# Optimization experiments

Measured on AMD Instinct MI355X. Metric: run time of the kernel, lower is better.

Reference implementation:

```python
import jax, jax.numpy as jnp
import numpy as np

N = 50000   # nodes
E = 800000  # edges (before self-loops)
IN = 128; H = 4; C = 32; HC = H * C; OUT = 47
EPS = 1e-16  # PyG softmax denominator eps
NEG_SLOPE = 0.2


def setup_inputs() -> dict:
    key = jax.random.key(0)
    ks = jax.random.split(key, 20)
    g = lambda k, shape, s=0.1: (jax.random.normal(k, shape, dtype=jnp.float32) * s)
    inp = {}
    inp["x"] = jax.random.normal(ks[0], (N, IN), dtype=jnp.float32)
    inp["edge_index"] = jax.random.randint(ks[1], (2, E), 0, N, dtype=jnp.int32)
    # layer 0: GATConv(IN -> H*C, concat=True) + skip Linear(IN -> HC)
    inp["lin_w0"] = g(ks[2], (IN, HC)); inp["att_src0"] = g(ks[3], (H, C)); inp["att_dst0"] = g(ks[4], (H, C))
    inp["bias0"] = g(ks[5], (HC,)); inp["skip_w0"] = g(ks[6], (IN, HC)); inp["skip_b0"] = g(ks[7], (HC,))
    # layer 1: GATConv(HC -> H*C, concat=True) + skip Linear(HC -> HC)
    inp["lin_w1"] = g(ks[8], (HC, HC)); inp["att_src1"] = g(ks[9], (H, C)); inp["att_dst1"] = g(ks[10], (H, C))
    inp["bias1"] = g(ks[11], (HC,)); inp["skip_w1"] = g(ks[12], (HC, HC)); inp["skip_b1"] = g(ks[13], (HC,))
    # layer 2: GATConv(HC -> OUT, heads=H, concat=False) + skip Linear(HC -> OUT)
    inp["lin_w2"] = g(ks[14], (HC, H * OUT)); inp["att_src2"] = g(ks[15], (H, OUT)); inp["att_dst2"] = g(ks[16], (H, OUT))
    inp["bias2"] = g(ks[17], (OUT,)); inp["skip_w2"] = g(ks[18], (HC, OUT)); inp["skip_b2"] = g(ks[19], (OUT,))
    return inp


def _gat_conv(x, src, dst, lin_w, att_src, att_dst, bias, concat):
    """PyG GATConv (self-loops already appended to src/dst)."""
    h, c = att_src.shape
    n = x.shape[0]
    xh = (x @ lin_w).reshape(n, h, c)                      # [N, H, C]
    a_src = jnp.einsum('nhc,hc->nh', xh, att_src)          # [N, H]
    a_dst = jnp.einsum('nhc,hc->nh', xh, att_dst)          # [N, H]
    e = a_src[src] + a_dst[dst]                            # [E', H]
    e = jax.nn.leaky_relu(e, NEG_SLOPE)
    # segment softmax over incoming edges per destination node
    m = jax.ops.segment_max(e, dst, num_segments=n)        # [N, H]
    ex = jnp.exp(e - m[dst])
    s = jax.ops.segment_sum(ex, dst, num_segments=n)       # [N, H]
    alpha = ex / (s[dst] + EPS)                            # [E', H]
    out = jax.ops.segment_sum(xh[src] * alpha[:, :, None], dst, num_segments=n)  # [N, H, C]
    out = out.reshape(n, h * c) if concat else out.mean(axis=1)
    return out + bias


def reference(x, edge_index, lin_w0, att_src0, att_dst0, bias0, skip_w0, skip_b0,
              lin_w1, att_src1, att_dst1, bias1, skip_w1, skip_b1,
              lin_w2, att_src2, att_dst2, bias2, skip_w2, skip_b2):
    n = x.shape[0]
    loop = jnp.arange(n, dtype=edge_index.dtype)
    src = jnp.concatenate([edge_index[0], loop])
    dst = jnp.concatenate([edge_index[1], loop])
    # layer 0 (+ skip, ELU; dropout is identity at inference)
    x = _gat_conv(x, src, dst, lin_w0, att_src0, att_dst0, bias0, True) + x @ skip_w0 + skip_b0
    x = jax.nn.elu(x)
    # layer 1
    x = _gat_conv(x, src, dst, lin_w1, att_src1, att_dst1, bias1, True) + x @ skip_w1 + skip_b1
    x = jax.nn.elu(x)
    # layer 2 (concat=False -> head mean), no activation
    x = _gat_conv(x, src, dst, lin_w2, att_src2, att_dst2, bias2, False) + x @ skip_w2 + skip_b2
    return x
```

## Files before the change

kernel.cpp:

```cpp
#include <hip/hip_runtime.h>
#include <math.h>
#include <type_traits>

#define KD 128
#define HC 128
#define NF2 188
#define NF2P 192
#define OUTC 47

typedef __attribute__((ext_vector_type(8))) __bf16 bf16x8;
typedef __attribute__((ext_vector_type(2))) __bf16 bf16x2;
typedef __attribute__((ext_vector_type(4))) float f32x4;

#ifdef __has_builtin
#if __has_builtin(__builtin_amdgcn_fdot2_f32_bf16)
#define HAVE_FDOT2 1
#endif
#endif

__device__ inline float bfhi_to_f(unsigned int u) {
    union { unsigned int u; float f; } c; c.u = u & 0xFFFF0000u; return c.f;
}
__device__ inline float bflo_to_f(unsigned int u) {
    union { unsigned int u; float f; } c; c.u = u << 16; return c.f;
}
__device__ inline unsigned short f_to_bfu(float f) {
    return __builtin_bit_cast(unsigned short, (__bf16)f);
}
__device__ inline unsigned int pk_bf(float a, float b) {
    return (unsigned int)f_to_bfu(a) | ((unsigned int)f_to_bfu(b) << 16);
}
__device__ inline float dot2pair(uint2 q, uint2 ab, float acc) {
#ifdef HAVE_FDOT2
    acc = __builtin_amdgcn_fdot2_f32_bf16(__builtin_bit_cast(bf16x2, q.x),
                                          __builtin_bit_cast(bf16x2, ab.x), acc, false);
    acc = __builtin_amdgcn_fdot2_f32_bf16(__builtin_bit_cast(bf16x2, q.y),
                                          __builtin_bit_cast(bf16x2, ab.y), acc, false);
#else
    acc += bflo_to_f(q.x) * bflo_to_f(ab.x) + bfhi_to_f(q.x) * bfhi_to_f(ab.x);
    acc += bflo_to_f(q.y) * bflo_to_f(ab.y) + bfhi_to_f(q.y) * bfhi_to_f(ab.y);
#endif
    return acc;
}

__global__ void init_deg_kernel(int* deg, int* counter, int n) {
    int i = blockIdx.x * blockDim.x + threadIdx.x;
    if (i < n) deg[i] = 1;
    if (i == 0) *counter = 0;
}

__global__ void count_kernel(const int* __restrict__ dst, int* deg, int e) {
    int t = blockIdx.x * blockDim.x + threadIdx.x;
    int base = t * 8;
    if (base + 7 < e) {
        int4 d0 = *(const int4*)(dst + base);
        int4 d1 = *(const int4*)(dst + base + 4);
        atomicAdd(&deg[d0.x], 1); atomicAdd(&deg[d0.y], 1);
        atomicAdd(&deg[d0.z], 1); atomicAdd(&deg[d0.w], 1);
        atomicAdd(&deg[d1.x], 1); atomicAdd(&deg[d1.y], 1);
        atomicAdd(&deg[d1.z], 1); atomicAdd(&deg[d1.w], 1);
    } else {
        for (int k = base; k < e; ++k) atomicAdd(&deg[dst[k]], 1);
    }
}

__global__ __launch_bounds__(256) void scan_base_kernel(
    const int* __restrict__ deg, int* counter,
    int* __restrict__ row_ptr, int* __restrict__ fill, int* __restrict__ col, int n) {
    int i = blockIdx.x * 256 + threadIdx.x;
    int v = (i < n) ? deg[i] : 0;
    int lane = threadIdx.x & 63, w = threadIdx.x >> 6;
    int incl = v;
#pragma unroll
    for (int off = 1; off < 64; off <<= 1) {
        int u = __shfl_up(incl, off, 64);
        if (lane >= off) incl += u;
    }
    __shared__ int wsum[4];
    __shared__ int base_sh;
    if (lane == 63) wsum[w] = incl;
    __syncthreads();
    if (threadIdx.x == 0)
        base_sh = atomicAdd(counter, wsum[0] + wsum[1] + wsum[2] + wsum[3]);
    int woff = 0;
    for (int k = 0; k < w; ++k) woff += wsum[k];
    __syncthreads();
    int excl = base_sh + woff + incl - v;
    if (i < n) {
        row_ptr[i] = excl;
        col[excl] = i;
        fill[i] = excl + 1;
    }
}

__global__ void fill_kernel(const int* __restrict__ ei, int* fill, int* col, int e) {
    int t = blockIdx.x * blockDim.x + threadIdx.x;
    int base = t * 8;
    if (base + 7 < e) {
        int4 s0 = *(const int4*)(ei + base);
        int4 s1 = *(const int4*)(ei + base + 4);
        int4 d0 = *(const int4*)(ei + e + base);
        int4 d1 = *(const int4*)(ei + e + base + 4);
        int p0 = atomicAdd(&fill[d0.x], 1);
        int p1 = atomicAdd(&fill[d0.y], 1);
        int p2 = atomicAdd(&fill[d0.z], 1);
        int p3 = atomicAdd(&fill[d0.w], 1);
        int p4 = atomicAdd(&fill[d1.x], 1);
        int p5 = atomicAdd(&fill[d1.y], 1);
        int p6 = atomicAdd(&fill[d1.z], 1);
        int p7 = atomicAdd(&fill[d1.w], 1);
        col[p0] = s0.x; col[p1] = s0.y; col[p2] = s0.z; col[p3] = s0.w;
        col[p4] = s1.x; col[p5] = s1.y; col[p6] = s1.z; col[p7] = s1.w;
    } else {
        for (int k = base; k < e; ++k) {
            int pos = atomicAdd(&fill[ei[e + k]], 1);
            col[pos] = ei[k];
        }
    }
}

template <typename AT, int NLIN, int NSK, int TR>
__global__ __launch_bounds__(256) void gemm_fused_kernel(
    const AT* __restrict__ A,
    const float* __restrict__ B0, __bf16* __restrict__ out0, int N0, int ldc0,
    const float* __restrict__ B1, const float* __restrict__ bias1,
    float* __restrict__ out1, int N1, int M) {
    __shared__ __bf16 As[64][136];
    __shared__ __bf16 Bs[64][136];
    int tid = threadIdx.x;
    int m0 = blockIdx.x * 64;

#pragma unroll
    for (int rep = 0; rep < 4; ++rep) {
        int idx = tid + rep * 256;
        int row = idx >> 4, seg = idx & 15;
        int gm = m0 + row;
        bf16x8 v = {};
        if (gm < M) {
            if constexpr (std::is_same<AT, float>::value) {
                const float* p = A + gm * KD + seg * 8;
                float4 f0 = *(const float4*)p;
                float4 f1 = *(const float4*)(p + 4);
                v[0] = (__bf16)f0.x; v[1] = (__bf16)f0.y; v[2] = (__bf16)f0.z; v[3] = (__bf16)f0.w;
                v[4] = (__bf16)f1.x; v[5] = (__bf16)f1.y; v[6] = (__bf16)f1.z; v[7] = (__bf16)f1.w;
            } else {
                v = *(const bf16x8*)(A + gm * KD + seg * 8);
            }
        }
        *(bf16x8*)&As[row][seg * 8] = v;
    }
    __syncthreads();

    int w = tid >> 6, lane = tid & 63;
    int lr = lane & 15, quad = lane >> 4;

#pragma unroll
    for (int t = 0; t < NLIN + NSK; ++t) {
        bool second = t >= NLIN;
        const float* B = second ? B1 : B0;
        int N = second ? N1 : N0;
        int n0 = (second ? (t - NLIN) : t) * 64;
        if (t) __syncthreads();
#pragma unroll
        for (int rep = 0; rep < 4; ++rep) {
            int idx = tid + rep * 256;
            int n = idx & 63, seg = idx >> 6;
            bf16x8 v = {};
            if (n0 + n < N) {
#pragma unroll
                for (int i = 0; i < 8; ++i) v[i] = (__bf16)B[(seg * 8 + i) * N + n0 + n];
            }
            *(bf16x8*)&Bs[n][seg * 8] = v;
        }
        __syncthreads();

        f32x4 acc[4] = {};
#pragma unroll
        for (int kc = 0; kc < 128; kc += 32) {
            bf16x8 a0 = *(const bf16x8*)&As[w * 16 + lr][kc + quad * 8];
            bf16x8 b0 = *(const bf16x8*)&Bs[lr][kc + quad * 8];
            bf16x8 b1 = *(const bf16x8*)&Bs[16 + lr][kc + quad * 8];
            bf16x8 b2 = *(const bf16x8*)&Bs[32 + lr][kc + quad * 8];
            bf16x8 b3 = *(const bf16x8*)&Bs[48 + lr][kc + quad * 8];
            acc[0] = __builtin_amdgcn_mfma_f32_16x16x32_bf16(a0, b0, acc[0], 0, 0, 0);
            acc[1] = __builtin_amdgcn_mfma_f32_16x16x32_bf16(a0, b1, acc[1], 0, 0, 0);
            acc[2] = __builtin_amdgcn_mfma_f32_16x16x32_bf16(a0, b2, acc[2], 0, 0, 0);
            acc[3] = __builtin_amdgcn_mfma_f32_16x16x32_bf16(a0, b3, acc[3], 0, 0, 0);
        }
#pragma unroll
        for (int c = 0; c < 4; ++c) {
#pragma unroll
            for (int reg = 0; reg < 4; ++reg) {
                int row = m0 + w * 16 + quad * 4 + reg;
                int colg = n0 + c * 16 + lr;
                if (row < M && colg < N) {
                    float v = acc[c][reg];
                    if (second) {
                        if (bias1) v += bias1[colg];
                        out1[row * N + colg] = v;
                    } else {
                        int idx;
                        if (TR) {
                            int h = (colg * 1395) >> 16;
                            idx = row * ldc0 + (colg - 47 * h) * 4 + h;
                        } else {
                            idx = row * ldc0 + colg;
                        }
                        out0[idx] = (__bf16)v;
                    }
                }
            }
        }
    }
}

__global__ __launch_bounds__(256) void att_kernel(
    const __bf16* __restrict__ xh, const float* __restrict__ att_s,
    const float* __restrict__ att_d, float* __restrict__ a_src,
    float* __restrict__ a_dst, int n) {
    int node = (blockIdx.x * blockDim.x + threadIdx.x) >> 6;
    int lane = threadIdx.x & 63;
    if (node >= n) return;
    float hs[4] = {0.f, 0.f, 0.f, 0.f};
    float hd[4] = {0.f, 0.f, 0.f, 0.f};
#pragma unroll
    for (int r = 0; r < 2; ++r) {
        int f = lane + 64 * r;
        float x = (float)xh[node * HC + f];
        float ps = x * att_s[f];
        float pd = x * att_d[f];
        int h = f >> 5;
        if (h == 0)      { hs[0] += ps; hd[0] += pd; }
        else if (h == 1) { hs[1] += ps; hd[1] += pd; }
        else if (h == 2) { hs[2] += ps; hd[2] += pd; }
        else             { hs[3] += ps; hd[3] += pd; }
    }
#pragma unroll
    for (int off = 32; off >= 1; off >>= 1) {
#pragma unroll
        for (int h = 0; h < 4; ++h) {
            hs[h] += __shfl_xor(hs[h], off, 64);
            hd[h] += __shfl_xor(hd[h], off, 64);
        }
    }
    if (lane == 0) {
        *(float4*)(a_src + 4 * node) = make_float4(hs[0], hs[1], hs[2], hs[3]);
        *(float4*)(a_dst + 4 * node) = make_float4(hd[0], hd[1], hd[2], hd[3]);
    }
}

__global__ __launch_bounds__(256) void att2_kernel(
    const __bf16* __restrict__ xh, const float* __restrict__ att_s,
    const float* __restrict__ att_d, float* __restrict__ a_src,
    float* __restrict__ a_dst, int n) {
    int node = (blockIdx.x * blockDim.x + threadIdx.x) >> 6;
    int lane = threadIdx.x & 63;
    if (node >= n) return;
    int h = lane & 3;
    float hs = 0.f, hd = 0.f;
#pragma unroll
    for (int r = 0; r < 3; ++r) {
        int f = lane + 64 * r;
        if (f < NF2) {
            float x = (float)xh[node * NF2P + f];
            int c = f >> 2;
            hs += x * att_s[h * 47 + c];
            hd += x * att_d[h * 47 + c];
        }
    }
#pragma unroll
    for (int off = 4; off <= 32; off <<= 1) {
        hs += __shfl_xor(hs, off, 64);
        hd += __shfl_xor(hd, off, 64);
    }
    if (lane < 4) {
        a_src[node * 4 + lane] = hs;
        a_dst[node * 4 + lane] = hd;
    }
}

template <int MODE>
__global__ __launch_bounds__(256) void agg_kernel(
    const __bf16* __restrict__ xh, const float* __restrict__ a_src,
    const float* __restrict__ a_dst, const float* __restrict__ skip,
    const float* __restrict__ bias, const int* __restrict__ row_ptr,
    const int* __restrict__ deg, const int* __restrict__ col,
    void* __restrict__ outp, int n) {
    __shared__ float s_af[4][64][4];
    __shared__ uint2 s_ab[4][64];
    __shared__ int s_j[4][64];
    int w = threadIdx.x >> 6;
    int lane = threadIdx.x & 63;
    int node = (blockIdx.x << 2) + w;
    bool active = node < n;
    int node_c = active ? node : 0;
    int start = row_ptr[node_c];
    int end = start + (active ? deg[node_c] : 0);
    float4 ad4 = *(const float4*)(a_dst + 4 * node_c);
    float adh[4] = {ad4.x, ad4.y, ad4.z, ad4.w};

    int e0 = start + lane;
    bool ok0 = e0 < end;
    int jcap = ok0 ? col[e0] : 0;
    float evc[4];
    {
        float4 as4 = *(const float4*)(a_src + 4 * jcap);
        float v0 = as4.x + adh[0]; evc[0] = v0 > 0.f ? v0 : 0.2f * v0;
        float v1 = as4.y + adh[1]; evc[1] = v1 > 0.f ? v1 : 0.2f * v1;
        float v2 = as4.z + adh[2]; evc[2] = v2 > 0.f ? v2 : 0.2f * v2;
        float v3 = as4.w + adh[3]; evc[3] = v3 > 0.f ? v3 : 0.2f * v3;
    }
    float m[4], s[4];
#pragma unroll
    for (int h = 0; h < 4; ++h) {
        m[h] = ok0 ? evc[h] : -1e30f;
        s[h] = ok0 ? 1.f : 0.f;
    }
    for (int e = e0 + 64; e < end; e += 64) {
        int j = col[e];
        float4 as4 = *(const float4*)(a_src + 4 * j);
        float ev[4] = {as4.x + adh[0], as4.y + adh[1], as4.z + adh[2], as4.w + adh[3]};
#pragma unroll
        for (int h = 0; h < 4; ++h) {
            float v = ev[h] > 0.f ? ev[h] : 0.2f * ev[h];
            float M = fmaxf(m[h], v);
            s[h] = s[h] * __expf(m[h] - M) + __expf(v - M);
            m[h] = M;
        }
    }
    float mloc[4];
#pragma unroll
    for (int h = 0; h < 4; ++h) mloc[h] = m[h];
#pragma unroll
    for (int off = 32; off >= 1; off >>= 1)
#pragma unroll
        for (int h = 0; h < 4; ++h) m[h] = fmaxf(m[h], __shfl_xor(m[h], off, 64));
#pragma unroll
    for (int h = 0; h < 4; ++h) s[h] *= __expf(mloc[h] - m[h]);
#pragma unroll
    for (int off = 32; off >= 1; off >>= 1)
#pragma unroll
        for (int h = 0; h < 4; ++h) s[h] += __shfl_xor(s[h], off, 64);
    float inv[4];
#pragma unroll
    for (int h = 0; h < 4; ++h) inv[h] = 1.f / (s[h] + 1e-16f);

    int half = lane >> 5, fl = lane & 31, myh2 = fl >> 3;
    bool lv = lane < 48;
    float acc0 = 0.f, acc1 = 0.f, acc2 = 0.f, acc3 = 0.f;
    const uint2* xb2 = (const uint2*)xh;
    uint2 zz = make_uint2(0u, 0u);

    auto run_chunk = [&](int cnt) {
        int t = 0;
        if (MODE == 0) {
            for (; t + 7 < cnt; t += 8) {
                int ja = s_j[w][t + half], jb = s_j[w][t + 2 + half];
                int jc = s_j[w][t + 4 + half], jd = s_j[w][t + 6 + half];
                uint2 qa = xb2[(ja << 5) + fl];
                uint2 qb = xb2[(jb << 5) + fl];
                uint2 qc = xb2[(jc << 5) + fl];
                uint2 qd = xb2[(jd << 5) + fl];
                float aa = s_af[w][t + half][myh2];
                float ab = s_af[w][t + 2 + half][myh2];
                float ac = s_af[w][t + 4 + half][myh2];
                float ad = s_af[w][t + 6 + half][myh2];
                acc0 += aa * bflo_to_f(qa.x); acc1 += aa * bfhi_to_f(qa.x);
                acc2 += aa * bflo_to_f(qa.y); acc3 += aa * bfhi_to_f(qa.y);
                acc0 += ab * bflo_to_f(qb.x); acc1 += ab * bfhi_to_f(qb.x);
                acc2 += ab * bflo_to_f(qb.y); acc3 += ab * bfhi_to_f(qb.y);
                acc0 += ac * bflo_to_f(qc.x); acc1 += ac * bfhi_to_f(qc.x);
                acc2 += ac * bflo_to_f(qc.y); acc3 += ac * bfhi_to_f(qc.y);
                acc0 += ad * bflo_to_f(qd.x); acc1 += ad * bfhi_to_f(qd.x);
                acc2 += ad * bflo_to_f(qd.y); acc3 += ad * bfhi_to_f(qd.y);
            }
            for (; t + 3 < cnt; t += 4) {
                int ja = s_j[w][t + half], jb = s_j[w][t + 2 + half];
                uint2 qa = xb2[(ja << 5) + fl];
                uint2 qb = xb2[(jb << 5) + fl];
                float aa = s_af[w][t + half][myh2];
                float ab = s_af[w][t + 2 + half][myh2];
                acc0 += aa * bflo_to_f(qa.x); acc1 += aa * bfhi_to_f(qa.x);
                acc2 += aa * bflo_to_f(qa.y); acc3 += aa * bfhi_to_f(qa.y);
                acc0 += ab * bflo_to_f(qb.x); acc1 += ab * bfhi_to_f(qb.x);
                acc2 += ab * bflo_to_f(qb.y); acc3 += ab * bfhi_to_f(qb.y);
            }
            for (; t + 1 < cnt; t += 2) {
                int j = s_j[w][t + half];
                uint2 q = xb2[(j << 5) + fl];
                float a = s_af[w][t + half][myh2];
                acc0 += a * bflo_to_f(q.x); acc1 += a * bfhi_to_f(q.x);
                acc2 += a * bflo_to_f(q.y); acc3 += a * bfhi_to_f(q.y);
            }
            for (; t < cnt; ++t) {
                int j = s_j[w][t];
                uint2 q = xb2[(j << 5) + fl];
                float a = (half == 0) ? s_af[w][t][myh2] : 0.f;
                acc0 += a * bflo_to_f(q.x); acc1 += a * bfhi_to_f(q.x);
                acc2 += a * bflo_to_f(q.y); acc3 += a * bfhi_to_f(q.y);
            }
        } else {
            for (; t + 7 < cnt; t += 8) {
                uint2 q0 = lv ? xb2[s_j[w][t] * 48 + lane] : zz;
                uint2 q1 = lv ? xb2[s_j[w][t + 1] * 48 + lane] : zz;
                uint2 q2 = lv ? xb2[s_j[w][t + 2] * 48 + lane] : zz;
                uint2 q3 = lv ? xb2[s_j[w][t + 3] * 48 + lane] : zz;
                uint2 q4 = lv ? xb2[s_j[w][t + 4] * 48 + lane] : zz;
                uint2 q5 = lv ? xb2[s_j[w][t + 5] * 48 + lane] : zz;
                uint2 q6 = lv ? xb2[s_j[w][t + 6] * 48 + lane] : zz;
                uint2 q7 = lv ? xb2[s_j[w][t + 7] * 48 + lane] : zz;
                acc0 = dot2pair(q0, s_ab[w][t], acc0);
                acc0 = dot2pair(q1, s_ab[w][t + 1], acc0);
                acc0 = dot2pair(q2, s_ab[w][t + 2], acc0);
                acc0 = dot2pair(q3, s_ab[w][t + 3], acc0);
                acc0 = dot2pair(q4, s_ab[w][t + 4], acc0);
                acc0 = dot2pair(q5, s_ab[w][t + 5], acc0);
                acc0 = dot2pair(q6, s_ab[w][t + 6], acc0);
                acc0 = dot2pair(q7, s_ab[w][t + 7], acc0);
            }
            for (; t + 3 < cnt; t += 4) {
                uint2 q0 = lv ? xb2[s_j[w][t] * 48 + lane] : zz;
                uint2 q1 = lv ? xb2[s_j[w][t + 1] * 48 + lane] : zz;
                uint2 q2 = lv ? xb2[s_j[w][t + 2] * 48 + lane] : zz;
                uint2 q3 = lv ? xb2[s_j[w][t + 3] * 48 + lane] : zz;
                acc0 = dot2pair(q0, s_ab[w][t], acc0);
                acc0 = dot2pair(q1, s_ab[w][t + 1], acc0);
                acc0 = dot2pair(q2, s_ab[w][t + 2], acc0);
                acc0 = dot2pair(q3, s_ab[w][t + 3], acc0);
            }
            for (; t < cnt; ++t) {
                uint2 q = lv ? xb2[s_j[w][t] * 48 + lane] : zz;
                acc0 = dot2pair(q, s_ab[w][t], acc0);
            }
        }
    };

    {
        float al[4];
#pragma unroll
        for (int h = 0; h < 4; ++h)
            al[h] = ok0 ? __expf(evc[h] - m[h]) * inv[h] : 0.f;
        s_j[w][lane] = jcap;
        if constexpr (MODE == 0)
            *(float4*)&s_af[w][lane][0] = make_float4(al[0], al[1], al[2], al[3]);
        else
            s_ab[w][lane] = make_uint2(pk_bf(al[0], al[1]), pk_bf(al[2], al[3]));
        int cnt = end - start; if (cnt > 64) cnt = 64;
        run_chunk(cnt);
    }
    for (int base = start + 64; base < end; base += 64) {
        int e = base + lane;
        bool ok = e < end;
        int jv = ok ? col[e] : 0;
        float4 as4 = *(const float4*)(a_src + 4 * jv);
        float asv[4] = {as4.x, as4.y, as4.z, as4.w};
        float al[4];
#pragma unroll
        for (int h = 0; h < 4; ++h) {
            float ev = asv[h] + adh[h];
            ev = ev > 0.f ? ev : 0.2f * ev;
            al[h] = ok ? __expf(ev - m[h]) * inv[h] : 0.f;
        }
        s_j[w][lane] = jv;
        if constexpr (MODE == 0)
            *(float4*)&s_af[w][lane][0] = make_float4(al[0], al[1], al[2], al[3]);
        else
            s_ab[w][lane] = make_uint2(pk_bf(al[0], al[1]), pk_bf(al[2], al[3]));
        int cnt = end - base; if (cnt > 64) cnt = 64;
        run_chunk(cnt);
    }

    if constexpr (MODE == 0) {
        acc0 += __shfl_xor(acc0, 32, 64);
        acc1 += __shfl_xor(acc1, 32, 64);
        acc2 += __shfl_xor(acc2, 32, 64);
        acc3 += __shfl_xor(acc3, 32, 64);
        if (active && half == 0) {
            float4 bb = *(const float4*)(bias + 4 * fl);
            float4 sk = *(const float4*)(skip + (node << 7) + 4 * fl);
            float v0 = acc0 + bb.x + sk.x;
            float v1 = acc1 + bb.y + sk.y;
            float v2 = acc2 + bb.z + sk.z;
            float v3 = acc3 + bb.w + sk.w;
            v0 = v0 > 0.f ? v0 : (__expf(v0) - 1.f);
            v1 = v1 > 0.f ? v1 : (__expf(v1) - 1.f);
            v2 = v2 > 0.f ? v2 : (__expf(v2) - 1.f);
            v3 = v3 > 0.f ? v3 : (__expf(v3) - 1.f);
            uint2 o = make_uint2(pk_bf(v0, v1), pk_bf(v2, v3));
            ((uint2*)outp)[(node << 5) + fl] = o;
        }
    } else {
        if (active && lane < OUTC) {
            float v = acc0 * 0.25f + bias[lane] + skip[node * OUTC + lane];
            ((float*)outp)[node * OUTC + lane] = v;
        }
    }
}

extern "C" void kernel_launch(void* const* d_in, const int* in_sizes, int n_in,
                              void* d_out, int out_size, void* d_ws, size_t ws_size,
                              hipStream_t stream) {
    const float* x        = (const float*)d_in[0];
    const int*   ei       = (const int*)d_in[1];
    const float* lin_w0   = (const float*)d_in[2];
    const float* att_src0 = (const float*)d_in[3];
    const float* att_dst0 = (const float*)d_in[4];
    const float* bias0    = (const float*)d_in[5];
    const float* skip_w0  = (const float*)d_in[6];
    const float* skip_b0  = (const float*)d_in[7];
    const float* lin_w1   = (const float*)d_in[8];
    const float* att_src1 = (const float*)d_in[9];
    const float* att_dst1 = (const float*)d_in[10];
    const float* bias1    = (const float*)d_in[11];
    const float* skip_w1  = (const float*)d_in[12];
    const float* skip_b1  = (const float*)d_in[13];
    const float* lin_w2   = (const float*)d_in[14];
    const float* att_src2 = (const float*)d_in[15];
    const float* att_dst2 = (const float*)d_in[16];
    const float* bias2    = (const float*)d_in[17];
    const float* skip_w2  = (const float*)d_in[18];
    const float* skip_b2  = (const float*)d_in[19];
    float* out = (float*)d_out;

    const int N = in_sizes[0] / KD;
    const int E = in_sizes[1] / 2;
    const int ET_ = E + N;

    char* ws = (char*)d_ws;
    size_t off = 0;
    auto alloc = [&](size_t bytes) -> void* {
        void* p = ws + off;
        off = (off + bytes + 255) & ~(size_t)255;
        return p;
    };
    __bf16* xh     = (__bf16*)alloc((size_t)N * NF2P * 2 + 256);
    __bf16* buf_bf = (__bf16*)alloc((size_t)N * HC * 2);
    float* skip    = (float*)alloc((size_t)N * HC * 4);
    float* a_src   = (float*)alloc((size_t)N * 4 * 4);
    float* a_dst   = (float*)alloc((size_t)N * 4 * 4);
    int* deg       = (int*)alloc((size_t)N * 4);
    int* row_ptr   = (int*)alloc((size_t)N * 4);
    int* fill      = (int*)alloc((size_t)N * 4);
    int* col       = (int*)alloc((size_t)ET_ * 4);
    int* counter   = (int*)alloc(256);

    init_deg_kernel<<<(N + 255) / 256, 256, 0, stream>>>(deg, counter, N);
    count_kernel<<<(E / 8 + 255) / 256, 256, 0, stream>>>(ei + E, deg, E);
    scan_base_kernel<<<(N + 255) / 256, 256, 0, stream>>>(deg, counter, row_ptr, fill, col, N);
    fill_kernel<<<(E / 8 + 255) / 256, 256, 0, stream>>>(ei, fill, col, E);

    dim3 blk(256);
    int mblocks = (N + 63) / 64;
    int wave_blocks = (N + 3) / 4;

    gemm_fused_kernel<float, 2, 2, 0><<<mblocks, blk, 0, stream>>>(
        x, lin_w0, xh, HC, HC, skip_w0, skip_b0, skip, HC, N);
    att_kernel<<<wave_blocks, blk, 0, stream>>>(xh, att_src0, att_dst0, a_src, a_dst, N);
    agg_kernel<0><<<wave_blocks, blk, 0, stream>>>(xh, a_src, a_dst, skip, bias0,
                                                   row_ptr, deg, col, buf_bf, N);
    gemm_fused_kernel<__bf16, 2, 2, 0><<<mblocks, blk, 0, stream>>>(
        buf_bf, lin_w1, xh, HC, HC, skip_w1, skip_b1, skip, HC, N);
    att_kernel<<<wave_blocks, blk, 0, stream>>>(xh, att_src1, att_dst1, a_src, a_dst, N);
    agg_kernel<0><<<wave_blocks, blk, 0, stream>>>(xh, a_src, a_dst, skip, bias1,
                                                   row_ptr, deg, col, buf_bf, N);
    gemm_fused_kernel<__bf16, 3, 1, 1><<<mblocks, blk, 0, stream>>>(
        buf_bf, lin_w2, xh, NF2, NF2P, skip_w2, skip_b2, skip, OUTC, N);
    att2_kernel<<<wave_blocks, blk, 0, stream>>>(xh, att_src2, att_dst2, a_src, a_dst, N);
    agg_kernel<1><<<wave_blocks, blk, 0, stream>>>(xh, a_src, a_dst, skip, bias2,
                                                   row_ptr, deg, col, out, N);
}
```

Measured before the change: 454.5 us.

## Store skip activations in bf16, narrow attention-score kernel, drop degree init kernel

The skip-connection output for layers 0 and 1 is now written and read as bf16 instead of fp32, halving that intermediate's memory traffic. The attention-score kernel maps 16 lanes per node with vectorized 16-byte loads instead of a full 64-lane wave, cutting the shuffle reductions. The degree-init kernel is replaced by memsets, and the self-loop +1 is folded into the scan kernel. The bf16 skip values add rounding error to the residual path.

New measurement: 410.6 us. 1.11x faster.

```diff
diff --git a/kernel.cpp b/kernel.cpp
--- a/kernel.cpp
+++ b/kernel.cpp
@@ -41,12 +41,6 @@
     acc += bflo_to_f(q.y) * bflo_to_f(ab.y) + bfhi_to_f(q.y) * bfhi_to_f(ab.y);
 #endif
     return acc;
-}
-
-__global__ void init_deg_kernel(int* deg, int* counter, int n) {
-    int i = blockIdx.x * blockDim.x + threadIdx.x;
-    if (i < n) deg[i] = 1;
-    if (i == 0) *counter = 0;
 }
 
 __global__ void count_kernel(const int* __restrict__ dst, int* deg, int e) {
@@ -65,10 +59,10 @@
 }
 
 __global__ __launch_bounds__(256) void scan_base_kernel(
-    const int* __restrict__ deg, int* counter,
+    int* __restrict__ deg, int* counter,
     int* __restrict__ row_ptr, int* __restrict__ fill, int* __restrict__ col, int n) {
     int i = blockIdx.x * 256 + threadIdx.x;
-    int v = (i < n) ? deg[i] : 0;
+    int v = (i < n) ? (deg[i] + 1) : 0;
     int lane = threadIdx.x & 63, w = threadIdx.x >> 6;
     int incl = v;
 #pragma unroll
@@ -90,6 +84,7 @@
         row_ptr[i] = excl;
         col[excl] = i;
         fill[i] = excl + 1;
+        deg[i] = v;
     }
 }
 
@@ -119,12 +114,12 @@
     }
 }
 
-template <typename AT, int NLIN, int NSK, int TR>
+template <typename AT, typename SKT, int NLIN, int NSK, int TR>
 __global__ __launch_bounds__(256) void gemm_fused_kernel(
     const AT* __restrict__ A,
     const float* __restrict__ B0, __bf16* __restrict__ out0, int N0, int ldc0,
     const float* __restrict__ B1, const float* __restrict__ bias1,
-    float* __restrict__ out1, int N1, int M) {
+    SKT* __restrict__ out1, int N1, int M) {
     __shared__ __bf16 As[64][136];
     __shared__ __bf16 Bs[64][136];
     int tid = threadIdx.x;
@@ -197,7 +192,7 @@
                     float v = acc[c][reg];
                     if (second) {
                         if (bias1) v += bias1[colg];
-                        out1[row * N + colg] = v;
+                        out1[row * N + colg] = (SKT)v;
                     } else {
                         int idx;
                         if (TR) {
@@ -218,34 +213,30 @@
     const __bf16* __restrict__ xh, const float* __restrict__ att_s,
     const float* __restrict__ att_d, float* __restrict__ a_src,
     float* __restrict__ a_dst, int n) {
-    int node = (blockIdx.x * blockDim.x + threadIdx.x) >> 6;
-    int lane = threadIdx.x & 63;
+    int tid = blockIdx.x * 256 + threadIdx.x;
+    int node = tid >> 4;
+    int l16 = threadIdx.x & 15;
     if (node >= n) return;
-    float hs[4] = {0.f, 0.f, 0.f, 0.f};
-    float hd[4] = {0.f, 0.f, 0.f, 0.f};
-#pragma unroll
-    for (int r = 0; r < 2; ++r) {
-        int f = lane + 64 * r;
-        float x = (float)xh[node * HC + f];
-        float ps = x * att_s[f];
-        float pd = x * att_d[f];
-        int h = f >> 5;
-        if (h == 0)      { hs[0] += ps; hd[0] += pd; }
-        else if (h == 1) { hs[1] += ps; hd[1] += pd; }
-        else if (h == 2) { hs[2] += ps; hd[2] += pd; }
-        else             { hs[3] += ps; hd[3] += pd; }
-    }
-#pragma unroll
-    for (int off = 32; off >= 1; off >>= 1) {
-#pragma unroll
-        for (int h = 0; h < 4; ++h) {
-            hs[h] += __shfl_xor(hs[h], off, 64);
-            hd[h] += __shfl_xor(hd[h], off, 64);
-        }
-    }
-    if (lane == 0) {
-        *(float4*)(a_src + 4 * node) = make_float4(hs[0], hs[1], hs[2], hs[3]);
-        *(float4*)(a_dst + 4 * node) = make_float4(hd[0], hd[1], hd[2], hd[3]);
+    uint4 q = ((const uint4*)xh)[node * 16 + l16];
+    int f0 = l16 * 8;
+    float4 as0 = *(const float4*)(att_s + f0);
+    float4 as1 = *(const float4*)(att_s + f0 + 4);
+    float4 ad0 = *(const float4*)(att_d + f0);
+    float4 ad1 = *(const float4*)(att_d + f0 + 4);
+    float x0 = bflo_to_f(q.x), x1 = bfhi_to_f(q.x);
+    float x2 = bflo_to_f(q.y), x3 = bfhi_to_f(q.y);
+    float x4 = bflo_to_f(q.z), x5 = bfhi_to_f(q.z);
+    float x6 = bflo_to_f(q.w), x7 = bfhi_to_f(q.w);
+    float hs = x0 * as0.x + x1 * as0.y + x2 * as0.z + x3 * as0.w
+             + x4 * as1.x + x5 * as1.y + x6 * as1.z + x7 * as1.w;
+    float hd = x0 * ad0.x + x1 * ad0.y + x2 * ad0.z + x3 * ad0.w
+             + x4 * ad1.x + x5 * ad1.y + x6 * ad1.z + x7 * ad1.w;
+    hs += __shfl_xor(hs, 1, 64); hs += __shfl_xor(hs, 2, 64);
+    hd += __shfl_xor(hd, 1, 64); hd += __shfl_xor(hd, 2, 64);
+    if ((l16 & 3) == 0) {
+        int h = l16 >> 2;
+        a_src[node * 4 + h] = hs;
+        a_dst[node * 4 + h] = hd;
     }
 }
 
@@ -282,7 +273,7 @@
 template <int MODE>
 __global__ __launch_bounds__(256) void agg_kernel(
     const __bf16* __restrict__ xh, const float* __restrict__ a_src,
-    const float* __restrict__ a_dst, const float* __restrict__ skip,
+    const float* __restrict__ a_dst, const void* __restrict__ skipp,
     const float* __restrict__ bias, const int* __restrict__ row_ptr,
     const int* __restrict__ deg, const int* __restrict__ col,
     void* __restrict__ outp, int n) {
@@ -477,11 +468,11 @@
         acc3 += __shfl_xor(acc3, 32, 64);
         if (active && half == 0) {
             float4 bb = *(const float4*)(bias + 4 * fl);
-            float4 sk = *(const float4*)(skip + (node << 7) + 4 * fl);
-            float v0 = acc0 + bb.x + sk.x;
-            float v1 = acc1 + bb.y + sk.y;
-            float v2 = acc2 + bb.z + sk.z;
-            float v3 = acc3 + bb.w + sk.w;
+            uint2 skq = ((const uint2*)skipp)[(node << 5) + fl];
+            float v0 = acc0 + bb.x + bflo_to_f(skq.x);
+            float v1 = acc1 + bb.y + bfhi_to_f(skq.x);
+            float v2 = acc2 + bb.z + bflo_to_f(skq.y);
+            float v3 = acc3 + bb.w + bfhi_to_f(skq.y);
             v0 = v0 > 0.f ? v0 : (__expf(v0) - 1.f);
             v1 = v1 > 0.f ? v1 : (__expf(v1) - 1.f);
             v2 = v2 > 0.f ? v2 : (__expf(v2) - 1.f);
@@ -491,6 +482,7 @@
         }
     } else {
         if (active && lane < OUTC) {
+            const float* skip = (const float*)skipp;
             float v = acc0 * 0.25f + bias[lane] + skip[node * OUTC + lane];
             ((float*)outp)[node * OUTC + lane] = v;
         }
@@ -533,18 +525,19 @@
         off = (off + bytes + 255) & ~(size_t)255;
         return p;
     };
-    __bf16* xh     = (__bf16*)alloc((size_t)N * NF2P * 2 + 256);
-    __bf16* buf_bf = (__bf16*)alloc((size_t)N * HC * 2);
-    float* skip    = (float*)alloc((size_t)N * HC * 4);
-    float* a_src   = (float*)alloc((size_t)N * 4 * 4);
-    float* a_dst   = (float*)alloc((size_t)N * 4 * 4);
-    int* deg       = (int*)alloc((size_t)N * 4);
-    int* row_ptr   = (int*)alloc((size_t)N * 4);
-    int* fill      = (int*)alloc((size_t)N * 4);
-    int* col       = (int*)alloc((size_t)ET_ * 4);
-    int* counter   = (int*)alloc(256);
-
-    init_deg_kernel<<<(N + 255) / 256, 256, 0, stream>>>(deg, counter, N);
+    __bf16* xh      = (__bf16*)alloc((size_t)N * NF2P * 2 + 256);
+    __bf16* buf_bf  = (__bf16*)alloc((size_t)N * HC * 2);
+    void*   skipbuf = alloc((size_t)N * HC * 4);
+    float* a_src    = (float*)alloc((size_t)N * 4 * 4);
+    float* a_dst    = (float*)alloc((size_t)N * 4 * 4);
+    int* deg        = (int*)alloc((size_t)N * 4);
+    int* row_ptr    = (int*)alloc((size_t)N * 4);
+    int* fill       = (int*)alloc((size_t)N * 4);
+    int* col        = (int*)alloc((size_t)ET_ * 4);
+    int* counter    = (int*)alloc(256);
+
+    hipMemsetAsync(deg, 0, (size_t)N * 4, stream);
+    hipMemsetAsync(counter, 0, 4, stream);
     count_kernel<<<(E / 8 + 255) / 256, 256, 0, stream>>>(ei + E, deg, E);
     scan_base_kernel<<<(N + 255) / 256, 256, 0, stream>>>(deg, counter, row_ptr, fill, col, N);
     fill_kernel<<<(E / 8 + 255) / 256, 256, 0, stream>>>(ei, fill, col, E);
@@ -552,20 +545,21 @@
     dim3 blk(256);
     int mblocks = (N + 63) / 64;
     int wave_blocks = (N + 3) / 4;
-
-    gemm_fused_kernel<float, 2, 2, 0><<<mblocks, blk, 0, stream>>>(
-        x, lin_w0, xh, HC, HC, skip_w0, skip_b0, skip, HC, N);
-    att_kernel<<<wave_blocks, blk, 0, stream>>>(xh, att_src0, att_dst0, a_src, a_dst, N);
-    agg_kernel<0><<<wave_blocks, blk, 0, stream>>>(xh, a_src, a_dst, skip, bias0,
+    int att_blocks = (N * 16 + 255) / 256;
+
+    gemm_fused_kernel<float, __bf16, 2, 2, 0><<<mblocks, blk, 0, stream>>>(
+        x, lin_w0, xh, HC, HC, skip_w0, skip_b0, (__bf16*)skipbuf, HC, N);
+    att_kernel<<<att_blocks, blk, 0, stream>>>(xh, att_src0, att_dst0, a_src, a_dst, N);
+    agg_kernel<0><<<wave_blocks, blk, 0, stream>>>(xh, a_src, a_dst, skipbuf, bias0,
                                                    row_ptr, deg, col, buf_bf, N);
-    gemm_fused_kernel<__bf16, 2, 2, 0><<<mblocks, blk, 0, stream>>>(
-        buf_bf, lin_w1, xh, HC, HC, skip_w1, skip_b1, skip, HC, N);
-    att_kernel<<<wave_blocks, blk, 0, stream>>>(xh, att_src1, att_dst1, a_src, a_dst, N);
-    agg_kernel<0><<<wave_blocks, blk, 0, stream>>>(xh, a_src, a_dst, skip, bias1,
+    gemm_fused_kernel<__bf16, __bf16, 2, 2, 0><<<mblocks, blk, 0, stream>>>(
+        buf_bf, lin_w1, xh, HC, HC, skip_w1, skip_b1, (__bf16*)skipbuf, HC, N);
+    att_kernel<<<att_blocks, blk, 0, stream>>>(xh, att_src1, att_dst1, a_src, a_dst, N);
+    agg_kernel<0><<<wave_blocks, blk, 0, stream>>>(xh, a_src, a_dst, skipbuf, bias1,
                                                    row_ptr, deg, col, buf_bf, N);
-    gemm_fused_kernel<__bf16, 3, 1, 1><<<mblocks, blk, 0, stream>>>(
-        buf_bf, lin_w2, xh, NF2, NF2P, skip_w2, skip_b2, skip, OUTC, N);
+    gemm_fused_kernel<__bf16, float, 3, 1, 1><<<mblocks, blk, 0, stream>>>(
+        buf_bf, lin_w2, xh, NF2, NF2P, skip_w2, skip_b2, (float*)skipbuf, OUTC, N);
     att2_kernel<<<wave_blocks, blk, 0, stream>>>(xh, att_src2, att_dst2, a_src, a_dst, N);
-    agg_kernel<1><<<wave_blocks, blk, 0, stream>>>(xh, a_src, a_dst, skip, bias2,
+    agg_kernel<1><<<wave_blocks, blk, 0, stream>>>(xh, a_src, a_dst, skipbuf, bias2,
                                                    row_ptr, deg, col, out, N);
 }
```
